# Performance work log

Hardware: AMD Instinct MI355X
Metric: run time of the kernel (lower is better)

The kernel has to match this reference:

```python
import jax, jax.numpy as jnp
import numpy as np

N = 100000       # nodes
E_RAND = 3200000  # random edges; + N self loops appended
F_IN = 128
D = 64
SUBHEADS = 2
ALPHA = 0.2  # leaky_relu negative slope


def setup_inputs() -> dict:
    key = jax.random.key(0)
    ks = jax.random.split(key, 8)
    x = jax.random.normal(ks[0], (N, F_IN), jnp.float32)
    src = jax.random.randint(ks[1], (E_RAND,), 0, N)
    dst = jax.random.randint(ks[2], (E_RAND,), 0, N)
    loops = jnp.arange(N)  # add_remaining_self_loops
    edge_index = jnp.stack([jnp.concatenate([src, loops]),
                            jnp.concatenate([dst, loops])])  # [2, E_RAND+N]
    # xavier_normal_(gain=1.414): std = gain*sqrt(2/(fan_in+fan_out))
    xav = lambda k, shp, fan: jax.random.normal(k, shp, jnp.float32) * np.float32(1.414 * np.sqrt(2.0 / fan))
    W = xav(ks[3], (SUBHEADS, F_IN, D), F_IN + D)     # per-subhead weight
    b = jnp.zeros((SUBHEADS, D), jnp.float32)          # per-subhead bias
    fc = xav(ks[4], (SUBHEADS, D, 1), D + 1)           # NodeAdaptiveEncoder.fc
    bf = jnp.zeros((SUBHEADS,), jnp.float32)           # NodeAdaptiveEncoder.bf
    a_src = xav(ks[5], (SUBHEADS, D), D + 1)           # attention vector (dst side)
    a_dst = xav(ks[6], (SUBHEADS, D), D + 1)           # attention vector (src side)
    return dict(x=x, edge_index=edge_index, W=W, b=b, fc=fc, bf=bf, a_src=a_src, a_dst=a_dst)


def reference(x, edge_index, W, b, fc, bf, a_src, a_dst):
    row, col = edge_index[0], edge_index[1]  # out[row] += val * h[col]
    n = x.shape[0]
    outs = []
    for i in range(SUBHEADS):
        h = x @ W[i]  # [N, D]; dropout is identity in eval mode
        # --- GAT-style edge attention over the sparse graph ---
        s_r = h @ a_src[i]  # [N]
        s_c = h @ a_dst[i]  # [N]
        e = jax.nn.leaky_relu(s_r[row] + s_c[col], ALPHA)  # [E]
        m = jax.ops.segment_max(e, row, num_segments=n)
        ee = jnp.exp(e - m[row])
        denom = jax.ops.segment_sum(ee, row, num_segments=n)
        att = ee / denom[row]  # adj_mat_val = ones * softmax(e)
        # --- row normalization ---
        rs = jax.ops.segment_sum(att, row, num_segments=n)
        val = att / jnp.where(rs == 0, 1.0, rs)[row]
        # --- (i+1) hops of spmm ---
        vh = h
        for _ in range(i + 1):
            vh = jax.ops.segment_sum(val[:, None] * vh[col], row, num_segments=n)
        vh = jnp.where(jnp.isnan(vh), 0.0, vh)  # val_h[val_h != val_h] = 0
        vh = vh + b[i]
        # --- NodeAdaptiveEncoder: relu(x) + sigmoid(x@fc+bf) * min(x, 0) ---
        g = jax.nn.sigmoid(vh @ fc[i] + bf[i])  # [N, 1]
        vh = jnp.maximum(vh, 0.0) + g * jnp.minimum(vh, 0.0)
        vh = jax.nn.leaky_relu(vh, ALPHA)  # activation
        outs.append(vh)
    return jnp.concatenate(outs, axis=1)  # [N, SUBHEADS*D]
```

## Files before the change

kernel.cpp:

```cpp
#include <hip/hip_runtime.h>

#define ALPHA 0.2f

__device__ __forceinline__ unsigned short f2bf(float f) {
    unsigned u = __float_as_uint(f);
    u += 0x7FFFu + ((u >> 16) & 1u);
    return (unsigned short)(u >> 16);
}
__device__ __forceinline__ float bflo(unsigned u) {
    return __uint_as_float(u << 16);
}
__device__ __forceinline__ float bfhi(unsigned u) {
    return __uint_as_float(u & 0xFFFF0000u);
}

__global__ __launch_bounds__(256) void f10_h(
    const float* __restrict__ x, const float* __restrict__ W,
    const float* __restrict__ a_src, const float* __restrict__ a_dst,
    const int* __restrict__ row, const int* __restrict__ col, int E,
    int* __restrict__ cnt,
    float* __restrict__ Hf, unsigned short* __restrict__ Hb,
    float* __restrict__ s_r, float* __restrict__ s_c, int N)
{
    __shared__ __align__(16) float ws[128][64];
    __shared__ __align__(16) float xs[128][36];
    const int t  = threadIdx.x;
    const int i  = blockIdx.x & 1;
    const int n0 = (blockIdx.x >> 1) * 32;

    if (cnt) {
        const long total = (long)gridDim.x * 256;
        for (long e = (long)blockIdx.x * 256 + t; e < E; e += total) {
            int r = row[e], c = col[e];
            if ((unsigned)r < (unsigned)N && (unsigned)c < (unsigned)N)
                atomicAdd(cnt + r, 1);
        }
    }

    {
        const float* wp = W + (size_t)i * 8192;
        #pragma unroll
        for (int j = 0; j < 8; ++j) {
            int idx = t + j * 256;
            int k   = idx >> 4;
            int c4  = (idx & 15) * 4;
            *(float4*)&ws[k][c4] = *(const float4*)(wp + k * 64 + c4);
        }
    }
    {
        int r = t >> 3;
        int n = n0 + r;
        #pragma unroll
        for (int j = 0; j < 4; ++j) {
            int k0 = ((t & 7) + j * 8) * 4;
            float4 v = (n < N) ? *(const float4*)(x + (size_t)n * 128 + k0)
                               : make_float4(0.f, 0.f, 0.f, 0.f);
            xs[k0 + 0][r] = v.x; xs[k0 + 1][r] = v.y;
            xs[k0 + 2][r] = v.z; xs[k0 + 3][r] = v.w;
        }
    }
    __syncthreads();

    const int tc = t & 31, tn = t >> 5;
    float acc[4][2] = {};
    #pragma unroll 8
    for (int k = 0; k < 128; ++k) {
        float4 xv = *(const float4*)&xs[k][tn * 4];
        float2 wv = *(const float2*)&ws[k][tc * 2];
        acc[0][0] = fmaf(xv.x, wv.x, acc[0][0]);
        acc[0][1] = fmaf(xv.x, wv.y, acc[0][1]);
        acc[1][0] = fmaf(xv.y, wv.x, acc[1][0]);
        acc[1][1] = fmaf(xv.y, wv.y, acc[1][1]);
        acc[2][0] = fmaf(xv.z, wv.x, acc[2][0]);
        acc[2][1] = fmaf(xv.z, wv.y, acc[2][1]);
        acc[3][0] = fmaf(xv.w, wv.x, acc[3][0]);
        acc[3][1] = fmaf(xv.w, wv.y, acc[3][1]);
    }

    const float2 asv = *(const float2*)(a_src + i * 64 + tc * 2);
    const float2 adv = *(const float2*)(a_dst + i * 64 + tc * 2);
    #pragma unroll
    for (int a = 0; a < 4; ++a) {
        int n = n0 + tn * 4 + a;
        if (n >= N) break;
        float2 hv; hv.x = acc[a][0]; hv.y = acc[a][1];
        if (Hf) *(float2*)(Hf + (size_t)n * 128 + i * 64 + tc * 2) = hv;
        if (Hb) {
            ushort2 hb; hb.x = f2bf(hv.x); hb.y = f2bf(hv.y);
            *(ushort2*)(Hb + (size_t)n * 128 + (i * 32 + tc) * 2) = hb;
        }
        float pr = hv.x * asv.x + hv.y * asv.y;
        float pc = hv.x * adv.x + hv.y * adv.y;
        #pragma unroll
        for (int off = 16; off; off >>= 1) {
            pr += __shfl_xor(pr, off);
            pc += __shfl_xor(pc, off);
        }
        if (tc == 0) {
            s_r[(size_t)i * N + n] = pr;
            s_c[(size_t)i * N + n] = pc;
        }
    }
}

__global__ __launch_bounds__(256) void f8_scan1(
    const int* __restrict__ cnt, int* __restrict__ bsums, int N)
{
    __shared__ int sdat[256];
    int t = threadIdx.x, b = blockIdx.x;
    int s = 0;
    #pragma unroll
    for (int j = 0; j < 4; ++j) {
        int idx = b * 1024 + t * 4 + j;
        if (idx < N) s += cnt[idx];
    }
    sdat[t] = s; __syncthreads();
    for (int o = 1; o < 256; o <<= 1) {
        int add = (t >= o) ? sdat[t - o] : 0;
        __syncthreads();
        sdat[t] += add;
        __syncthreads();
    }
    if (t == 255) bsums[b] = sdat[255];
}
__global__ __launch_bounds__(256) void f8_scan2(
    const int* __restrict__ bsums, int* __restrict__ boffs, int nb)
{
    __shared__ int sdat[256];
    int t = threadIdx.x;
    int v = (t < nb) ? bsums[t] : 0;
    sdat[t] = v; __syncthreads();
    for (int o = 1; o < 256; o <<= 1) {
        int add = (t >= o) ? sdat[t - o] : 0;
        __syncthreads();
        sdat[t] += add;
        __syncthreads();
    }
    if (t < nb) boffs[t] = sdat[t] - v;
}
__global__ __launch_bounds__(256) void f11_scan3(
    int* __restrict__ cnt, const int* __restrict__ boffs,
    int* __restrict__ rp, int N)
{
    __shared__ int sdat[256];
    int t = threadIdx.x, b = blockIdx.x;
    int v[4]; int s = 0;
    #pragma unroll
    for (int j = 0; j < 4; ++j) {
        int idx = b * 1024 + t * 4 + j;
        v[j] = (idx < N) ? cnt[idx] : 0;
        s += v[j];
    }
    sdat[t] = s; __syncthreads();
    for (int o = 1; o < 256; o <<= 1) {
        int add = (t >= o) ? sdat[t - o] : 0;
        __syncthreads();
        sdat[t] += add;
        __syncthreads();
    }
    int excl = boffs[b] + sdat[t] - s;
    #pragma unroll
    for (int j = 0; j < 4; ++j) {
        int idx = b * 1024 + t * 4 + j;
        if (idx < N) {
            rp[idx]  = excl;
            cnt[idx] = excl;
            if (idx == N - 1) rp[N] = excl + v[j];
            excl += v[j];
        }
    }
}

__global__ __launch_bounds__(256) void f12_scatter(
    const int* __restrict__ row, const int* __restrict__ col, int E,
    const float* __restrict__ s_r, const float* __restrict__ s_c,
    int* __restrict__ cur, uint2* __restrict__ pk, int N)
{
    int e = blockIdx.x * 256 + threadIdx.x;
    if (e >= E) return;
    int r = row[e], c = col[e];
    if ((unsigned)r >= (unsigned)N || (unsigned)c >= (unsigned)N) return;
    int pos = atomicAdd(cur + r, 1);
    float e0 = s_r[r] + s_c[c];
    float e1 = s_r[(size_t)N + r] + s_c[(size_t)N + c];
    e0 = (e0 > 0.f) ? e0 : ALPHA * e0;
    e1 = (e1 > 0.f) ? e1 : ALPHA * e1;
    unsigned py = ((unsigned)f2bf(expf(e1)) << 16) | (unsigned)f2bf(expf(e0));
    uint2 m; m.x = (unsigned)c; m.y = py;
    pk[pos] = m;
}

__global__ __launch_bounds__(256) void f12_spmm2(
    const int* __restrict__ rp, const uint2* __restrict__ pk,
    const unsigned* __restrict__ Hb,
    const float* __restrict__ b, const float* __restrict__ fc,
    const float* __restrict__ bfv,
    unsigned short* __restrict__ A1b, float* __restrict__ out, int N)
{
    long gid = (long)blockIdx.x * 256 + threadIdx.x;
    int r = (int)(gid >> 6), d = (int)(gid & 63);
    if (r >= N) return;
    int p0 = rp[r], p1 = rp[r + 1];
    const int sub = d >> 5;
    float a0 = 0.f, a1 = 0.f, den = 0.f;
    int p = p0;
    for (; p + 8 <= p1; p += 8) {
        uint2 m0 = pk[p],     m1 = pk[p + 1], m2 = pk[p + 2], m3 = pk[p + 3];
        uint2 m4 = pk[p + 4], m5 = pk[p + 5], m6 = pk[p + 6], m7 = pk[p + 7];
        unsigned u0 = Hb[(size_t)m0.x * 64 + d];
        unsigned u1 = Hb[(size_t)m1.x * 64 + d];
        unsigned u2 = Hb[(size_t)m2.x * 64 + d];
        unsigned u3 = Hb[(size_t)m3.x * 64 + d];
        unsigned u4 = Hb[(size_t)m4.x * 64 + d];
        unsigned u5 = Hb[(size_t)m5.x * 64 + d];
        unsigned u6 = Hb[(size_t)m6.x * 64 + d];
        unsigned u7 = Hb[(size_t)m7.x * 64 + d];
        float v0 = sub ? bfhi(m0.y) : bflo(m0.y);
        float v1 = sub ? bfhi(m1.y) : bflo(m1.y);
        float v2 = sub ? bfhi(m2.y) : bflo(m2.y);
        float v3 = sub ? bfhi(m3.y) : bflo(m3.y);
        float v4 = sub ? bfhi(m4.y) : bflo(m4.y);
        float v5 = sub ? bfhi(m5.y) : bflo(m5.y);
        float v6 = sub ? bfhi(m6.y) : bflo(m6.y);
        float v7 = sub ? bfhi(m7.y) : bflo(m7.y);
        a0 = fmaf(v0, bflo(u0), a0); a1 = fmaf(v0, bfhi(u0), a1); den += v0;
        a0 = fmaf(v1, bflo(u1), a0); a1 = fmaf(v1, bfhi(u1), a1); den += v1;
        a0 = fmaf(v2, bflo(u2), a0); a1 = fmaf(v2, bfhi(u2), a1); den += v2;
        a0 = fmaf(v3, bflo(u3), a0); a1 = fmaf(v3, bfhi(u3), a1); den += v3;
        a0 = fmaf(v4, bflo(u4), a0); a1 = fmaf(v4, bfhi(u4), a1); den += v4;
        a0 = fmaf(v5, bflo(u5), a0); a1 = fmaf(v5, bfhi(u5), a1); den += v5;
        a0 = fmaf(v6, bflo(u6), a0); a1 = fmaf(v6, bfhi(u6), a1); den += v6;
        a0 = fmaf(v7, bflo(u7), a0); a1 = fmaf(v7, bfhi(u7), a1); den += v7;
    }
    for (; p < p1; ++p) {
        uint2 m = pk[p];
        unsigned u = Hb[(size_t)m.x * 64 + d];
        float v = sub ? bfhi(m.y) : bflo(m.y);
        a0 = fmaf(v, bflo(u), a0); a1 = fmaf(v, bfhi(u), a1); den += v;
    }
    float inv = (p1 > p0) ? 1.f / den : 0.f;
    float r0 = a0 * inv, r1 = a1 * inv;
    if (sub) {
        ushort2 res; res.x = f2bf(r0); res.y = f2bf(r1);
        *(ushort2*)(A1b + (size_t)r * 64 + (d - 32) * 2) = res;
    } else {
        int dcol = 2 * d;
        float vh0 = (r0 != r0) ? 0.f : r0;
        float vh1 = (r1 != r1) ? 0.f : r1;
        float2 bb = *(const float2*)(b + dcol);
        float2 ff = *(const float2*)(fc + dcol);
        vh0 += bb.x; vh1 += bb.y;
        float pp = vh0 * ff.x + vh1 * ff.y;
        #pragma unroll
        for (int off = 16; off; off >>= 1) pp += __shfl_xor(pp, off);
        float g = 1.f / (1.f + expf(-(pp + bfv[0])));
        float q0 = fmaxf(vh0, 0.f) + g * fminf(vh0, 0.f);
        float q1 = fmaxf(vh1, 0.f) + g * fminf(vh1, 0.f);
        q0 = (q0 > 0.f) ? q0 : ALPHA * q0;
        q1 = (q1 > 0.f) ? q1 : ALPHA * q1;
        float2 res; res.x = q0; res.y = q1;
        *(float2*)(out + (size_t)r * 128 + dcol) = res;
    }
}

__global__ __launch_bounds__(256) void f12_fin2(
    const int* __restrict__ rp, const uint2* __restrict__ pk,
    const unsigned short* __restrict__ A1b,
    const float* __restrict__ b, const float* __restrict__ fc,
    const float* __restrict__ bfv,
    float* __restrict__ out, int N)
{
    long gid = (long)blockIdx.x * 256 + threadIdx.x;
    int r = (int)(gid >> 6), d = (int)(gid & 63);
    if (r >= N) return;
    int p0 = rp[r], p1 = rp[r + 1];
    float acc = 0.f, den = 0.f;
    int p = p0;
    for (; p + 8 <= p1; p += 8) {
        uint2 m0 = pk[p],     m1 = pk[p + 1], m2 = pk[p + 2], m3 = pk[p + 3];
        uint2 m4 = pk[p + 4], m5 = pk[p + 5], m6 = pk[p + 6], m7 = pk[p + 7];
        float s0 = bflo(A1b[(size_t)m0.x * 64 + d]);
        float s1 = bflo(A1b[(size_t)m1.x * 64 + d]);
        float s2 = bflo(A1b[(size_t)m2.x * 64 + d]);
        float s3 = bflo(A1b[(size_t)m3.x * 64 + d]);
        float s4 = bflo(A1b[(size_t)m4.x * 64 + d]);
        float s5 = bflo(A1b[(size_t)m5.x * 64 + d]);
        float s6 = bflo(A1b[(size_t)m6.x * 64 + d]);
        float s7 = bflo(A1b[(size_t)m7.x * 64 + d]);
        float v0 = bfhi(m0.y), v1 = bfhi(m1.y), v2 = bfhi(m2.y), v3 = bfhi(m3.y);
        float v4 = bfhi(m4.y), v5 = bfhi(m5.y), v6 = bfhi(m6.y), v7 = bfhi(m7.y);
        acc = fmaf(v0, s0, acc); den += v0;
        acc = fmaf(v1, s1, acc); den += v1;
        acc = fmaf(v2, s2, acc); den += v2;
        acc = fmaf(v3, s3, acc); den += v3;
        acc = fmaf(v4, s4, acc); den += v4;
        acc = fmaf(v5, s5, acc); den += v5;
        acc = fmaf(v6, s6, acc); den += v6;
        acc = fmaf(v7, s7, acc); den += v7;
    }
    for (; p < p1; ++p) {
        uint2 m = pk[p];
        float v = bfhi(m.y);
        acc = fmaf(v, bflo(A1b[(size_t)m.x * 64 + d]), acc); den += v;
    }
    float vh = (p1 > p0) ? acc / den : 0.f;
    if (vh != vh) vh = 0.f;
    vh += b[64 + d];
    float pp = vh * fc[64 + d];
    #pragma unroll
    for (int off = 32; off; off >>= 1) pp += __shfl_xor(pp, off);
    float g = 1.f / (1.f + expf(-(pp + bfv[1])));
    float res = fmaxf(vh, 0.f) + g * fminf(vh, 0.f);
    res = (res > 0.f) ? res : ALPHA * res;
    out[(size_t)r * 128 + 64 + d] = res;
}

__global__ __launch_bounds__(256) void f8_scatter(
    const int* __restrict__ row, const int* __restrict__ col, int E,
    int* __restrict__ cur, int* __restrict__ colp, int N)
{
    int e = blockIdx.x * 256 + threadIdx.x;
    if (e >= E) return;
    int r = row[e], c = col[e];
    if ((unsigned)r >= (unsigned)N || (unsigned)c >= (unsigned)N) return;
    int pos = atomicAdd(cur + r, 1);
    colp[pos] = c;
}

__global__ __launch_bounds__(256) void f11_spmm2_cp(
    const int* __restrict__ rp, const int* __restrict__ colp,
    const float* __restrict__ s_r, const float* __restrict__ s_c,
    const float* __restrict__ H,
    float* __restrict__ A0, float* __restrict__ A1, int N)
{
    long gid = (long)blockIdx.x * 256 + threadIdx.x;
    int r = (int)(gid >> 6), d = (int)(gid & 63);
    if (r >= N) return;
    int p0 = rp[r], p1 = rp[r + 1];
    const int sub = d >> 5;
    const float* scp = s_c + (size_t)sub * N;
    float sr = s_r[(size_t)sub * N + r];
    const float2* H2 = (const float2*)H;
    float a0 = 0.f, a1 = 0.f, den = 0.f;
    int p = p0;
    for (; p + 4 <= p1; p += 4) {
        int c0 = colp[p], c1 = colp[p + 1], c2 = colp[p + 2], c3 = colp[p + 3];
        float sc0 = scp[c0], sc1 = scp[c1], sc2 = scp[c2], sc3 = scp[c3];
        float2 h0 = H2[(size_t)c0 * 64 + d];
        float2 h1 = H2[(size_t)c1 * 64 + d];
        float2 h2 = H2[(size_t)c2 * 64 + d];
        float2 h3 = H2[(size_t)c3 * 64 + d];
        float e0 = sr + sc0; e0 = (e0 > 0.f) ? e0 : ALPHA * e0; float v0 = expf(e0);
        float e1 = sr + sc1; e1 = (e1 > 0.f) ? e1 : ALPHA * e1; float v1 = expf(e1);
        float e2 = sr + sc2; e2 = (e2 > 0.f) ? e2 : ALPHA * e2; float v2 = expf(e2);
        float e3 = sr + sc3; e3 = (e3 > 0.f) ? e3 : ALPHA * e3; float v3 = expf(e3);
        a0 = fmaf(v0, h0.x, a0); a1 = fmaf(v0, h0.y, a1); den += v0;
        a0 = fmaf(v1, h1.x, a0); a1 = fmaf(v1, h1.y, a1); den += v1;
        a0 = fmaf(v2, h2.x, a0); a1 = fmaf(v2, h2.y, a1); den += v2;
        a0 = fmaf(v3, h3.x, a0); a1 = fmaf(v3, h3.y, a1); den += v3;
    }
    for (; p < p1; ++p) {
        int c = colp[p];
        float e0 = sr + scp[c];
        e0 = (e0 > 0.f) ? e0 : ALPHA * e0;
        float v = expf(e0);
        float2 h = H2[(size_t)c * 64 + d];
        a0 = fmaf(v, h.x, a0); a1 = fmaf(v, h.y, a1); den += v;
    }
    float inv = (p1 > p0) ? 1.f / den : 0.f;
    int dcol = (2 * d) & 63;
    float2 res; res.x = a0 * inv; res.y = a1 * inv;
    float* dst = sub ? A1 : A0;
    *(float2*)(dst + (size_t)r * 64 + dcol) = res;
}

__global__ __launch_bounds__(256) void f9_spmm_fin(
    const int* __restrict__ rp, const int* __restrict__ colp,
    const float* __restrict__ s_r, const float* __restrict__ s_c,
    const float* __restrict__ src, int ss, int soff,
    const float* __restrict__ b, const float* __restrict__ fc,
    const float* __restrict__ bfv,
    float* __restrict__ out, int N, int sub)
{
    long gid = (long)blockIdx.x * 256 + threadIdx.x;
    int r = (int)(gid >> 6), d = (int)(gid & 63);
    if (r >= N) return;
    int p0 = rp[r], p1 = rp[r + 1];
    float sr = s_r[r];
    float acc = 0.f, den = 0.f;
    int p = p0;
    for (; p + 4 <= p1; p += 4) {
        int c0 = colp[p], c1 = colp[p + 1], c2 = colp[p + 2], c3 = colp[p + 3];
        float sc0 = s_c[c0], sc1 = s_c[c1], sc2 = s_c[c2], sc3 = s_c[c3];
        float s0 = src[(size_t)c0 * ss + soff + d];
        float s1 = src[(size_t)c1 * ss + soff + d];
        float s2 = src[(size_t)c2 * ss + soff + d];
        float s3 = src[(size_t)c3 * ss + soff + d];
        float e0 = sr + sc0; e0 = (e0 > 0.f) ? e0 : ALPHA * e0; float v0 = expf(e0);
        float e1 = sr + sc1; e1 = (e1 > 0.f) ? e1 : ALPHA * e1; float v1 = expf(e1);
        float e2 = sr + sc2; e2 = (e2 > 0.f) ? e2 : ALPHA * e2; float v2 = expf(e2);
        float e3 = sr + sc3; e3 = (e3 > 0.f) ? e3 : ALPHA * e3; float v3 = expf(e3);
        acc = fmaf(v0, s0, acc); den += v0;
        acc = fmaf(v1, s1, acc); den += v1;
        acc = fmaf(v2, s2, acc); den += v2;
        acc = fmaf(v3, s3, acc); den += v3;
    }
    for (; p < p1; ++p) {
        int c = colp[p];
        float ev = sr + s_c[c];
        ev = (ev > 0.f) ? ev : ALPHA * ev;
        float v = expf(ev);
        acc = fmaf(v, src[(size_t)c * ss + soff + d], acc);
        den += v;
    }
    float vh = (p1 > p0) ? acc / den : 0.f;
    if (vh != vh) vh = 0.f;
    vh += b[sub * 64 + d];
    float pp = vh * fc[sub * 64 + d];
    #pragma unroll
    for (int off = 32; off; off >>= 1) pp += __shfl_xor(pp, off);
    float g = 1.f / (1.f + expf(-(pp + bfv[sub])));
    float res = fmaxf(vh, 0.f) + g * fminf(vh, 0.f);
    res = (res > 0.f) ? res : ALPHA * res;
    out[(size_t)r * 128 + sub * 64 + d] = res;
}

__global__ __launch_bounds__(256) void f8_fin(
    const float* __restrict__ A,
    const float* __restrict__ b, const float* __restrict__ fc,
    const float* __restrict__ bfv,
    float* __restrict__ out, int N, int sub)
{
    long gid = (long)blockIdx.x * 256 + threadIdx.x;
    int n = (int)(gid >> 6), d = (int)(gid & 63);
    if (n >= N) return;
    float vh = A[(size_t)n * 64 + d];
    if (vh != vh) vh = 0.f;
    vh += b[sub * 64 + d];
    float p = vh * fc[sub * 64 + d];
    #pragma unroll
    for (int off = 32; off; off >>= 1) p += __shfl_xor(p, off);
    float g = 1.f / (1.f + expf(-(p + bfv[sub])));
    float res = fmaxf(vh, 0.f) + g * fminf(vh, 0.f);
    res = (res > 0.f) ? res : ALPHA * res;
    out[(size_t)n * 128 + sub * 64 + d] = res;
}

__global__ __launch_bounds__(256) void f8_edge(
    const int* __restrict__ row, const int* __restrict__ col, int E,
    const float* __restrict__ s_r, const float* __restrict__ s_c,
    float* __restrict__ denom, int* __restrict__ cnt, int N)
{
    int e = blockIdx.x * 256 + threadIdx.x;
    if (e >= E) return;
    int r = row[e], c = col[e];
    if ((unsigned)r >= (unsigned)N || (unsigned)c >= (unsigned)N) return;
    if (cnt) atomicAdd(cnt + r, 1);
    #pragma unroll
    for (int i = 0; i < 2; ++i) {
        float ev = s_r[(size_t)i * N + r] + s_c[(size_t)i * N + c];
        ev = (ev > 0.f) ? ev : ALPHA * ev;
        atomicAdd(denom + (size_t)i * N + r, expf(ev));
    }
}
__global__ __launch_bounds__(256) void f7_spmm(
    const int* __restrict__ row, const int* __restrict__ col, int E,
    const float* __restrict__ s_r, const float* __restrict__ s_c,
    const float* __restrict__ denom,
    const float* __restrict__ out, int hcol,
    float* __restrict__ A, int N)
{
    long gid = (long)blockIdx.x * 256 + threadIdx.x;
    long wv  = gid >> 6;
    int  d   = (int)(gid & 63);
    long e0 = wv * 8, e1 = e0 + 8; if (e1 > E) e1 = E;
    for (long e = e0; e < e1; ++e) {
        int r = row[e], c = col[e];
        if ((unsigned)r >= (unsigned)N || (unsigned)c >= (unsigned)N) continue;
        float ev = s_r[r] + s_c[c];
        ev = (ev > 0.f) ? ev : ALPHA * ev;
        float v = expf(ev) / denom[r];
        atomicAdd(A + (size_t)r * 64 + d, v * out[(size_t)c * 128 + hcol + d]);
    }
}
__global__ __launch_bounds__(256) void f7_copy(
    const float* __restrict__ A, float* __restrict__ out, int cbase, int N)
{
    long gid = (long)blockIdx.x * 256 + threadIdx.x;
    long n = gid >> 6; int d = (int)(gid & 63);
    if (n >= N) return;
    out[(size_t)n * 128 + cbase + d] = A[(size_t)n * 64 + d];
}

extern "C" void kernel_launch(void* const* d_in, const int* in_sizes, int n_in,
                              void* d_out, int out_size, void* d_ws, size_t ws_size,
                              hipStream_t stream) {
    const float* x     = (const float*)d_in[0];
    const int*   ei    = (const int*)d_in[1];
    const float* W     = (const float*)d_in[2];
    const float* b     = (const float*)d_in[3];
    const float* fc    = (const float*)d_in[4];
    const float* bfv   = (const float*)d_in[5];
    const float* a_src = (const float*)d_in[6];
    const float* a_dst = (const float*)d_in[7];
    float* out = (float*)d_out;

    const int N = in_sizes[0] / 128;
    const int E = in_sizes[1] / 2;
    const int* row = ei;
    const int* col = ei + E;
    (void)n_in; (void)out_size;

    unsigned short* Hb   = (unsigned short*)d_ws;
    unsigned short* A1b  = Hb + (size_t)N * 128;
    uint2*          pk   = (uint2*)(A1b + (size_t)N * 64);
    float*          s_rP = (float*)(pk + E);
    float*          s_cP = s_rP + 2 * (size_t)N;
    int*            rpP  = (int*)(s_cP + 2 * (size_t)N);
    int*            cntP = rpP + (N + 1);
    int*            bsumP = cntP + N;
    int*            boffP = bsumP + 256;
    size_t          needP = (size_t)((char*)(boffP + 256) - (char*)d_ws);

    float* A0a   = (float*)d_ws;
    float* A1a   = A0a + (size_t)N * 64;
    int*   colpA = (int*)(A1a + (size_t)N * 64);
    float* s_rA  = (float*)(colpA + E);
    float* s_cA  = s_rA + 2 * (size_t)N;
    int*   rpA   = (int*)(s_cA + 2 * (size_t)N);
    int*   cntA  = rpA + (N + 1);
    int*   bsumA = cntA + N;
    int*   boffA = bsumA + 256;
    size_t needA = (size_t)((char*)(boffA + 256) - (char*)d_ws);

    const int g10 = 2 * ((N + 31) / 32);
    const int eb  = (E + 255) / 256;
    const int rb  = (int)(((long)N * 64 + 255) / 256);
    const int nb  = (N + 1023) / 1024;

    if (ws_size >= needP) {
        hipMemsetAsync(cntP, 0, (size_t)N * sizeof(int), stream);
        f10_h<<<g10, 256, 0, stream>>>(x, W, a_src, a_dst, row, col, E, cntP,
                                       nullptr, Hb, s_rP, s_cP, N);
        f8_scan1<<<nb, 256, 0, stream>>>(cntP, bsumP, N);
        f8_scan2<<<1, 256, 0, stream>>>(bsumP, boffP, nb);
        f11_scan3<<<nb, 256, 0, stream>>>(cntP, boffP, rpP, N);
        f12_scatter<<<eb, 256, 0, stream>>>(row, col, E, s_rP, s_cP, cntP, pk, N);
        f12_spmm2<<<rb, 256, 0, stream>>>(rpP, pk, (const unsigned*)Hb,
                                          b, fc, bfv, A1b, out, N);
        f12_fin2<<<rb, 256, 0, stream>>>(rpP, pk, A1b, b, fc, bfv, out, N);
    } else if (ws_size >= needA) {
        hipMemsetAsync(cntA, 0, (size_t)N * sizeof(int), stream);
        f10_h<<<g10, 256, 0, stream>>>(x, W, a_src, a_dst, row, col, E, cntA,
                                       out, nullptr, s_rA, s_cA, N);
        f8_scan1<<<nb, 256, 0, stream>>>(cntA, bsumA, N);
        f8_scan2<<<1, 256, 0, stream>>>(bsumA, boffA, nb);
        f11_scan3<<<nb, 256, 0, stream>>>(cntA, boffA, rpA, N);
        f8_scatter<<<eb, 256, 0, stream>>>(row, col, E, cntA, colpA, N);
        f11_spmm2_cp<<<rb, 256, 0, stream>>>(rpA, colpA, s_rA, s_cA, out,
                                             A0a, A1a, N);
        f8_fin<<<rb, 256, 0, stream>>>(A0a, b, fc, bfv, out, N, 0);
        f9_spmm_fin<<<rb, 256, 0, stream>>>(rpA, colpA, s_rA + N, s_cA + N,
                                            A1a, 64, 0, b, fc, bfv, out, N, 1);
    } else {
        float* A     = (float*)d_ws;
        float* s_r   = A + (size_t)N * 64;
        float* s_c   = s_r + 2 * (size_t)N;
        float* denom = s_c + 2 * (size_t)N;
        const size_t planeB = (size_t)N * 64 * sizeof(float);
        const int sb = (int)(((((long)E + 7) / 8) * 64 + 255) / 256);
        hipMemsetAsync(denom, 0, 2 * (size_t)N * sizeof(float), stream);
        f10_h<<<g10, 256, 0, stream>>>(x, W, a_src, a_dst, row, col, E, nullptr,
                                       out, nullptr, s_r, s_c, N);
        f8_edge<<<eb, 256, 0, stream>>>(row, col, E, s_r, s_c, denom, nullptr, N);
        const float* s_r1 = s_r + N; const float* s_c1 = s_c + N; const float* den1 = denom + N;
        hipMemsetAsync(A, 0, planeB, stream);
        f7_spmm<<<sb, 256, 0, stream>>>(row, col, E, s_r, s_c, denom, out, 0, A, N);
        f8_fin<<<rb, 256, 0, stream>>>(A, b, fc, bfv, out, N, 0);
        hipMemsetAsync(A, 0, planeB, stream);
        f7_spmm<<<sb, 256, 0, stream>>>(row, col, E, s_r1, s_c1, den1, out, 64, A, N);
        f7_copy<<<rb, 256, 0, stream>>>(A, out, 64, N);
        hipMemsetAsync(A, 0, planeB, stream);
        f7_spmm<<<sb, 256, 0, stream>>>(row, col, E, s_r1, s_c1, den1, out, 64, A, N);
        f8_fin<<<rb, 256, 0, stream>>>(A, b, fc, bfv, out, N, 1);
    }
}
```

Before: 632.4 us.

## Compute node projection with bf16 MFMA after a separate conversion pass

Replaces the FP32 LDS-tiled projection kernel with two kernels. The first converts x and a transposed W to bf16 while also doing the degree-count atomics. The second computes H = xW with 16x16x32 bf16 MFMA instructions and derives the attention scores s_r and s_c from the accumulators with lane shuffles. This cuts the ALU cost of the GEMM but adds a full bf16 copy of x in workspace, an extra kernel launch, and lower-precision attention scores.

```diff
diff --git a/kernel.cpp b/kernel.cpp
--- a/kernel.cpp
+++ b/kernel.cpp
@@ -1,6 +1,9 @@
 #include <hip/hip_runtime.h>
 
 #define ALPHA 0.2f
+
+typedef short bf16x8 __attribute__((ext_vector_type(8)));
+typedef float f32x4  __attribute__((ext_vector_type(4)));
 
 __device__ __forceinline__ unsigned short f2bf(float f) {
     unsigned u = __float_as_uint(f);
@@ -12,6 +15,107 @@
 }
 __device__ __forceinline__ float bfhi(unsigned u) {
     return __uint_as_float(u & 0xFFFF0000u);
+}
+
+__global__ __launch_bounds__(256) void f13_cvt(
+    const float* __restrict__ x, const float* __restrict__ W,
+    const int* __restrict__ row, const int* __restrict__ col, int E,
+    int* __restrict__ cnt,
+    unsigned short* __restrict__ xb, unsigned short* __restrict__ WT,
+    long total8, int N)
+{
+    long gid = (long)blockIdx.x * 256 + threadIdx.x;
+    const long total = (long)gridDim.x * 256;
+    for (long e = gid; e < E; e += total) {
+        int r = row[e], c = col[e];
+        if ((unsigned)r < (unsigned)N && (unsigned)c < (unsigned)N)
+            atomicAdd(cnt + r, 1);
+    }
+    for (long t = gid; t < total8; t += total) {
+        const float4* xp = (const float4*)(x + t * 8);
+        float4 v0 = xp[0], v1 = xp[1];
+        uint4 o;
+        o.x = ((unsigned)f2bf(v0.y) << 16) | f2bf(v0.x);
+        o.y = ((unsigned)f2bf(v0.w) << 16) | f2bf(v0.z);
+        o.z = ((unsigned)f2bf(v1.y) << 16) | f2bf(v1.x);
+        o.w = ((unsigned)f2bf(v1.w) << 16) | f2bf(v1.z);
+        *(uint4*)(xb + t * 8) = o;
+    }
+    for (long t = gid; t < 2 * 64 * 128; t += total) {
+        int i = (int)(t >> 13);
+        int c = (int)((t >> 7) & 63);
+        int k = (int)(t & 127);
+        WT[t] = f2bf(W[i * 8192 + k * 64 + c]);
+    }
+}
+
+__global__ __launch_bounds__(256) void f13_h(
+    const unsigned short* __restrict__ xb,
+    const unsigned short* __restrict__ WT,
+    const float* __restrict__ a_src, const float* __restrict__ a_dst,
+    unsigned short* __restrict__ Hb,
+    float* __restrict__ s_r, float* __restrict__ s_c, int N)
+{
+    const int t  = threadIdx.x;
+    const int wv = t >> 6, l = t & 63;
+    const int i  = blockIdx.x & 1;
+    const int n0 = (blockIdx.x >> 1) * 64 + wv * 16;
+    const int lm = l & 15, lg = l >> 4;
+
+    int arow = n0 + lm; if (arow >= N) arow = N - 1;
+    const unsigned short* xr = xb + (size_t)arow * 128 + lg * 8;
+    bf16x8 af[4];
+    #pragma unroll
+    for (int ks = 0; ks < 4; ++ks)
+        af[ks] = *(const bf16x8*)(xr + ks * 32);
+
+    const unsigned short* wr = WT + ((size_t)i * 64 + lm) * 128 + lg * 8;
+    f32x4 zero = {0.f, 0.f, 0.f, 0.f};
+    f32x4 acc[4];
+    #pragma unroll
+    for (int ct = 0; ct < 4; ++ct) {
+        acc[ct] = zero;
+        #pragma unroll
+        for (int ks = 0; ks < 4; ++ks) {
+            bf16x8 bf = *(const bf16x8*)(wr + ct * 16 * 128 + ks * 32);
+            acc[ct] = __builtin_amdgcn_mfma_f32_16x16x32_bf16(af[ks], bf, acc[ct], 0, 0, 0);
+        }
+    }
+
+    float asv[4], adv[4];
+    #pragma unroll
+    for (int ct = 0; ct < 4; ++ct) {
+        asv[ct] = a_src[i * 64 + ct * 16 + lm];
+        adv[ct] = a_dst[i * 64 + ct * 16 + lm];
+    }
+    #pragma unroll
+    for (int reg = 0; reg < 4; ++reg) {
+        float vr = 0.f, vc = 0.f;
+        #pragma unroll
+        for (int ct = 0; ct < 4; ++ct) {
+            vr = fmaf(acc[ct][reg], asv[ct], vr);
+            vc = fmaf(acc[ct][reg], adv[ct], vc);
+        }
+        #pragma unroll
+        for (int off = 8; off; off >>= 1) {
+            vr += __shfl_xor(vr, off);
+            vc += __shfl_xor(vc, off);
+        }
+        int n = n0 + lg * 4 + reg;
+        if (lm == 0 && n < N) {
+            s_r[(size_t)i * N + n] = vr;
+            s_c[(size_t)i * N + n] = vc;
+        }
+    }
+
+    #pragma unroll
+    for (int reg = 0; reg < 4; ++reg) {
+        int n = n0 + lg * 4 + reg;
+        if (n >= N) continue;
+        #pragma unroll
+        for (int ct = 0; ct < 4; ++ct)
+            Hb[(size_t)n * 128 + i * 64 + ct * 16 + lm] = f2bf(acc[ct][reg]);
+    }
 }
 
 __global__ __launch_bounds__(256) void f10_h(
@@ -36,7 +140,6 @@
                 atomicAdd(cnt + r, 1);
         }
     }
-
     {
         const float* wp = W + (size_t)i * 8192;
         #pragma unroll
@@ -188,6 +291,18 @@
     unsigned py = ((unsigned)f2bf(expf(e1)) << 16) | (unsigned)f2bf(expf(e0));
     uint2 m; m.x = (unsigned)c; m.y = py;
     pk[pos] = m;
+}
+
+__global__ __launch_bounds__(256) void f8_scatter(
+    const int* __restrict__ row, const int* __restrict__ col, int E,
+    int* __restrict__ cur, int* __restrict__ colp, int N)
+{
+    int e = blockIdx.x * 256 + threadIdx.x;
+    if (e >= E) return;
+    int r = row[e], c = col[e];
+    if ((unsigned)r >= (unsigned)N || (unsigned)c >= (unsigned)N) return;
+    int pos = atomicAdd(cur + r, 1);
+    colp[pos] = c;
 }
 
 __global__ __launch_bounds__(256) void f12_spmm2(
@@ -315,18 +430,6 @@
     out[(size_t)r * 128 + 64 + d] = res;
 }
 
-__global__ __launch_bounds__(256) void f8_scatter(
-    const int* __restrict__ row, const int* __restrict__ col, int E,
-    int* __restrict__ cur, int* __restrict__ colp, int N)
-{
-    int e = blockIdx.x * 256 + threadIdx.x;
-    if (e >= E) return;
-    int r = row[e], c = col[e];
-    if ((unsigned)r >= (unsigned)N || (unsigned)c >= (unsigned)N) return;
-    int pos = atomicAdd(cur + r, 1);
-    colp[pos] = c;
-}
-
 __global__ __launch_bounds__(256) void f11_spmm2_cp(
     const int* __restrict__ rp, const int* __restrict__ colp,
     const float* __restrict__ s_r, const float* __restrict__ s_c,
@@ -511,9 +614,11 @@
     const int* col = ei + E;
     (void)n_in; (void)out_size;
 
-    unsigned short* Hb   = (unsigned short*)d_ws;
+    unsigned short* xb   = (unsigned short*)d_ws;
+    unsigned short* Hb   = xb + (size_t)N * 128;
     unsigned short* A1b  = Hb + (size_t)N * 128;
-    uint2*          pk   = (uint2*)(A1b + (size_t)N * 64);
+    unsigned short* WT   = A1b + (size_t)N * 64;
+    uint2*          pk   = (uint2*)(WT + 16384);
     float*          s_rP = (float*)(pk + E);
     float*          s_cP = s_rP + 2 * (size_t)N;
     int*            rpP  = (int*)(s_cP + 2 * (size_t)N);
@@ -534,14 +639,18 @@
     size_t needA = (size_t)((char*)(boffA + 256) - (char*)d_ws);
 
     const int g10 = 2 * ((N + 31) / 32);
+    const int g13 = 2 * ((N + 63) / 64);
+    const long total8 = (long)N * 128 / 8;
+    const int gcv = (int)((total8 + 255) / 256);
     const int eb  = (E + 255) / 256;
     const int rb  = (int)(((long)N * 64 + 255) / 256);
     const int nb  = (N + 1023) / 1024;
 
     if (ws_size >= needP) {
         hipMemsetAsync(cntP, 0, (size_t)N * sizeof(int), stream);
-        f10_h<<<g10, 256, 0, stream>>>(x, W, a_src, a_dst, row, col, E, cntP,
-                                       nullptr, Hb, s_rP, s_cP, N);
+        f13_cvt<<<gcv, 256, 0, stream>>>(x, W, row, col, E, cntP, xb, WT,
+                                         total8, N);
+        f13_h<<<g13, 256, 0, stream>>>(xb, WT, a_src, a_dst, Hb, s_rP, s_cP, N);
         f8_scan1<<<nb, 256, 0, stream>>>(cntP, bsumP, N);
         f8_scan2<<<1, 256, 0, stream>>>(bsumP, boffP, nb);
         f11_scan3<<<nb, 256, 0, stream>>>(cntP, boffP, rpP, N);
```

New measurement: 647.4 us. 2.4% more time.
